# Optimization experiments

Hardware: AMD Instinct MI355X
Metric: run time of the kernel (lower is better)

The kernel has to match this reference:

```python
import jax, jax.numpy as jnp
import numpy as np

N, E, D = 40000, 320000, 128          # nodes, edges, model dim
H, C = 4, 128                          # GAT heads, per-head channels
DEPTH, MLP = 2, 512
NEG_SLOPE = 0.2
EPS_SM = 1e-16                         # PyG softmax denom epsilon


def layer_norm(x, g, b):
    mu = jnp.mean(x, axis=-1, keepdims=True)
    var = jnp.var(x, axis=-1, keepdims=True)
    return (x - mu) * jax.lax.rsqrt(var + 1e-5) * g + b


def gat_conv(x, src, dst, edge_attr, W, a_src, a_dst, We, a_edge, bias):
    # x: [N,D]; W: [D,H*C]; a_*: [H,C]; We: [1,H*C]; bias: [H*C]
    h = (x @ W).reshape(N, H, C)                       # [N,H,C]
    alpha_src = jnp.einsum('nhc,hc->nh', h, a_src)      # [N,H]
    alpha_dst = jnp.einsum('nhc,hc->nh', h, a_dst)      # [N,H]
    e = (edge_attr @ We).reshape(E, H, C)               # [E,H,C]
    alpha_e = jnp.einsum('ehc,hc->eh', e, a_edge)       # [E,H]
    alpha = alpha_src[src] + alpha_dst[dst] + alpha_e   # [E,H]
    alpha = jax.nn.leaky_relu(alpha, NEG_SLOPE)
    # segment softmax over edges sharing the same destination node
    amax = jax.ops.segment_max(alpha, dst, num_segments=N)   # [N,H]
    ex = jnp.exp(alpha - amax[dst])                          # [E,H]
    denom = jax.ops.segment_sum(ex, dst, num_segments=N)     # [N,H]
    attn = ex / (denom[dst] + EPS_SM)                        # [E,H]
    # message = attn * x_j ; aggregate by destination (scatter-add)
    msg = attn[:, :, None] * h[src]                          # [E,H,C]
    out = jax.ops.segment_sum(msg, dst, num_segments=N)      # [N,H,C]
    return out.reshape(N, H * C) + bias                      # concat heads


def setup_inputs():
    key = jax.random.key(0)
    ks = jax.random.split(key, 16)
    s = 0.05
    f32 = jnp.float32
    inp = {
        'x': jax.random.normal(ks[0], (N, D), f32),
        'edge_index': jax.random.randint(ks[1], (2, E), 0, N),
        'edge_attr': jax.random.normal(ks[2], (E, 1), f32),
        'ln1_g': jnp.ones((DEPTH, D), f32),
        'ln1_b': jnp.zeros((DEPTH, D), f32),
        'gat_W': jax.random.normal(ks[3], (DEPTH, D, H * C), f32) * s,
        'att_src': jax.random.normal(ks[4], (DEPTH, H, C), f32) * s,
        'att_dst': jax.random.normal(ks[5], (DEPTH, H, C), f32) * s,
        'edge_W': jax.random.normal(ks[6], (DEPTH, 1, H * C), f32) * s,
        'att_edge': jax.random.normal(ks[7], (DEPTH, H, C), f32) * s,
        'gat_bias': jnp.zeros((DEPTH, H * C), f32),
        'qf_W': jax.random.normal(ks[8], (DEPTH, H * C, D), f32) * s,
        'qf_b': jnp.zeros((DEPTH, D), f32),
        'ln2_g': jnp.ones((DEPTH, D), f32),
        'ln2_b': jnp.zeros((DEPTH, D), f32),
        'ff_W1': jax.random.normal(ks[9], (DEPTH, D, MLP), f32) * s,
        'ff_b1': jnp.zeros((DEPTH, MLP), f32),
        'ff_W2': jax.random.normal(ks[10], (DEPTH, MLP, D), f32) * s,
        'ff_b2': jnp.zeros((DEPTH, D), f32),
    }
    return inp


def reference(x, edge_index, edge_attr, ln1_g, ln1_b, gat_W, att_src, att_dst,
              edge_W, att_edge, gat_bias, qf_W, qf_b, ln2_g, ln2_b,
              ff_W1, ff_b1, ff_W2, ff_b2):
    src, dst = edge_index[0], edge_index[1]
    for d in range(DEPTH):
        # Residual(PreNorm(QuickFix(GATConv)))
        h = layer_norm(x, ln1_g[d], ln1_b[d])
        g = gat_conv(h, src, dst, edge_attr, gat_W[d], att_src[d], att_dst[d],
                     edge_W[d], att_edge[d], gat_bias[d])
        x = x + g @ qf_W[d] + qf_b[d]
        # Residual(PreNorm(FeedForward))
        h = layer_norm(x, ln2_g[d], ln2_b[d])
        x = x + jax.nn.gelu(h @ ff_W1[d] + ff_b1[d]) @ ff_W2[d] + ff_b2[d]
    return x
```

## Files before the change

kernel.cpp:

```cpp
#include <hip/hip_runtime.h>
#include <hip/hip_bf16.h>

#define N_NODES 40000
#define M_PAD   40064
#define N_EDGES 320000
#define DIM 128
#define HC 512
#define NHEAD 4
#define CHEAD 128
#define DEPTH_L 2
#define MLP_DIM 512
#define SCAN_NB ((N_NODES + 255) / 256)

typedef __attribute__((ext_vector_type(8))) short short8;
typedef __attribute__((ext_vector_type(4))) float f32x4;

static __device__ __forceinline__ void gload_lds16(const void* g, void* l)
{
    __builtin_amdgcn_global_load_lds(
        (const __attribute__((address_space(1))) unsigned int*)g,
        (__attribute__((address_space(3))) unsigned int*)l,
        16, 0, 0);
}

static __device__ __forceinline__ unsigned int packbf2(float a, float b)
{
    union { __hip_bfloat16 h[2]; unsigned int u; } p;
    p.h[0] = __float2bfloat16(a);
    p.h[1] = __float2bfloat16(b);
    return p.u;
}

static __device__ __forceinline__ float gelu_f(float v)
{
    float z2 = -1.5957691216f * (v + 0.044715f * v * v * v);
    return v / (1.f + __expf(z2));
}

__global__ __launch_bounds__(256) void k_ln(const float* __restrict__ x,
                                            const float* __restrict__ gma,
                                            const float* __restrict__ bta,
                                            __hip_bfloat16* __restrict__ out, int M)
{
    int row = blockIdx.x * 4 + (threadIdx.x >> 6);
    int lane = threadIdx.x & 63;
    if (row >= M) return;
    float2 v = *reinterpret_cast<const float2*>(x + (size_t)row * DIM + lane * 2);
    float s = v.x + v.y, sq = v.x * v.x + v.y * v.y;
    #pragma unroll
    for (int d = 32; d; d >>= 1) { s += __shfl_xor(s, d); sq += __shfl_xor(sq, d); }
    float mean = s * (1.f / DIM);
    float var = sq * (1.f / DIM) - mean * mean;
    float rs = rsqrtf(var + 1e-5f);
    int c = lane * 2;
    union { __hip_bfloat16 b[2]; unsigned int u; } p;
    p.b[0] = __float2bfloat16((v.x - mean) * rs * gma[c] + bta[c]);
    p.b[1] = __float2bfloat16((v.y - mean) * rs * gma[c + 1] + bta[c + 1]);
    *reinterpret_cast<unsigned int*>(out + (size_t)row * DIM + c) = p.u;
}

struct WcvtArgs {
    const float* src[4];
    __hip_bfloat16* dst[4];
    int K[4];
    int Nn[4];
};
__global__ __launch_bounds__(256) void k_wcvt4(WcvtArgs a)
{
    int j = blockIdx.y;
    int i = blockIdx.x * 256 + threadIdx.x;
    int K = a.K[j], N = a.Nn[j];
    if (i < K * N) {
        int n = i / K, k = i % K;
        a.dst[j][i] = __float2bfloat16(a.src[j][(size_t)k * N + n]);
    }
}

__global__ void k_prep_u(const float* __restrict__ gat_W,
                         const float* __restrict__ att_src,
                         const float* __restrict__ att_dst,
                         float* __restrict__ uvec)
{
    int b = blockIdx.x;
    int d = b >> 3, t8 = b & 7;
    int t = t8 >> 2, h = t8 & 3;
    int c = threadIdx.x;
    const float* W = gat_W + (size_t)d * DIM * HC;
    const float* av = (t == 0 ? att_src : att_dst) + (size_t)d * NHEAD * CHEAD + h * CHEAD;
    float s = 0.f;
    for (int cc = 0; cc < CHEAD; ++cc)
        s += W[(size_t)c * HC + h * CHEAD + cc] * av[cc];
    uvec[(size_t)d * 1024 + t8 * 128 + c] = s;
}

__global__ __launch_bounds__(256) void k_prep_m(const float* __restrict__ gat_W,
                                                const float* __restrict__ qf_W,
                                                __hip_bfloat16* __restrict__ Mt)
{
    int i = blockIdx.x * 256 + threadIdx.x;
    int d = i >> 16;
    int hk = (i >> 7) & 511;
    int j = i & 127;
    int h = hk >> 7, k = hk & 127;
    const float* W = gat_W + (size_t)d * DIM * HC + (size_t)k * HC + h * CHEAD;
    const float* Q = qf_W + (size_t)d * HC * DIM + (size_t)h * CHEAD * DIM + j;
    float s = 0.f;
    for (int c = 0; c < CHEAD; ++c)
        s += W[c] * Q[(size_t)c * DIM];
    Mt[(size_t)d * 65536 + (size_t)j * 512 + hk] = __float2bfloat16(s);
}

__global__ __launch_bounds__(256) void k_prep_c(const float* __restrict__ gat_bias,
                                                const float* __restrict__ qf_W,
                                                const float* __restrict__ qf_b,
                                                float* __restrict__ cvec)
{
    int idx = blockIdx.x * 4 + (threadIdx.x >> 6);
    int lane = threadIdx.x & 63;
    int d = idx >> 7, j = idx & 127;
    float s = 0.f;
    for (int m = lane; m < HC; m += 64)
        s += gat_bias[(size_t)d * HC + m] * qf_W[(size_t)d * HC * DIM + (size_t)m * DIM + j];
    #pragma unroll
    for (int dd = 32; dd; dd >>= 1) s += __shfl_xor(s, dd);
    if (lane == 0) cvec[idx] = s + qf_b[(size_t)d * DIM + j];
}

__global__ void k_ae(const float* __restrict__ We, const float* __restrict__ a_edge,
                     float* __restrict__ ae)
{
    int d = blockIdx.x;
    int h = threadIdx.x >> 6, lane = threadIdx.x & 63;
    float2 w = *reinterpret_cast<const float2*>(We + (size_t)d * HC + h * CHEAD + lane * 2);
    float2 a = *reinterpret_cast<const float2*>(a_edge + (size_t)d * NHEAD * CHEAD + h * CHEAD + lane * 2);
    float s = w.x * a.x + w.y * a.y;
    #pragma unroll
    for (int dd = 32; dd; dd >>= 1) s += __shfl_xor(s, dd);
    if (lane == 0) ae[d * 4 + h] = s;
}

__global__ __launch_bounds__(256) void k_dots(const unsigned int* __restrict__ hln,
                                              const float* __restrict__ uvec,
                                              float* __restrict__ asrc,
                                              float* __restrict__ adst)
{
    int n = blockIdx.x * 4 + (threadIdx.x >> 6);
    int lane = threadIdx.x & 63;
    unsigned int u = hln[n * 64 + lane];
    float f0 = __uint_as_float(u << 16);
    float f1 = __uint_as_float(u & 0xffff0000u);
    float s[8];
    #pragma unroll
    for (int t = 0; t < 8; ++t) {
        float2 uv = *reinterpret_cast<const float2*>(uvec + t * 128 + lane * 2);
        s[t] = f0 * uv.x + f1 * uv.y;
    }
    #pragma unroll
    for (int d = 32; d; d >>= 1) {
        #pragma unroll
        for (int t = 0; t < 8; ++t) s[t] += __shfl_xor(s[t], d);
    }
    if (lane == 0) {
        reinterpret_cast<float4*>(asrc)[n] = make_float4(s[0], s[1], s[2], s[3]);
        reinterpret_cast<float4*>(adst)[n] = make_float4(s[4], s[5], s[6], s[7]);
    }
}

__global__ __launch_bounds__(256) void k_alpha(const int* __restrict__ scsr,
                                               const int* __restrict__ dcsr,
                                               const float* __restrict__ eacsr,
                                               const float* __restrict__ asrc,
                                               const float* __restrict__ adst,
                                               const float* __restrict__ ae4v,
                                               float* __restrict__ wcsr)
{
    int p = blockIdx.x * 256 + threadIdx.x;
    if (p >= N_EDGES) return;
    int s = scsr[p], dd = dcsr[p];
    float q = eacsr[p];
    float4 as = reinterpret_cast<const float4*>(asrc)[s];
    float4 ad = reinterpret_cast<const float4*>(adst)[dd];
    float4 ae = *reinterpret_cast<const float4*>(ae4v);
    float4 w;
    float al;
    al = as.x + ad.x + ae.x * q; al = al > 0.f ? al : 0.2f * al; w.x = __expf(al);
    al = as.y + ad.y + ae.y * q; al = al > 0.f ? al : 0.2f * al; w.y = __expf(al);
    al = as.z + ad.z + ae.z * q; al = al > 0.f ? al : 0.2f * al; w.z = __expf(al);
    al = as.w + ad.w + ae.w * q; al = al > 0.f ? al : 0.2f * al; w.w = __expf(al);
    reinterpret_cast<float4*>(wcsr)[p] = w;
}

__global__ __launch_bounds__(256) void k_agg2(const int* __restrict__ off,
                                              const int* __restrict__ scsr,
                                              const float* __restrict__ wcsr,
                                              const unsigned int* __restrict__ hln,
                                              unsigned int* __restrict__ agg)
{
    int n = blockIdx.x * 4 + (threadIdx.x >> 6);
    int lane = threadIdx.x & 63;
    int e0 = off[n], e1 = off[n + 1];
    float den[4] = {0, 0, 0, 0};
    float accA[4] = {0, 0, 0, 0};
    float accB[4] = {0, 0, 0, 0};
    int i = e0;
    for (; i + 1 < e1; i += 2) {
        int s0 = scsr[i], s1 = scsr[i + 1];
        float4 w0 = reinterpret_cast<const float4*>(wcsr)[i];
        float4 w1 = reinterpret_cast<const float4*>(wcsr)[i + 1];
        unsigned int u0 = hln[s0 * 64 + lane];
        unsigned int u1 = hln[s1 * 64 + lane];
        float f00 = __uint_as_float(u0 << 16);
        float f01 = __uint_as_float(u0 & 0xffff0000u);
        float f10 = __uint_as_float(u1 << 16);
        float f11 = __uint_as_float(u1 & 0xffff0000u);
        den[0] += w0.x + w1.x; den[1] += w0.y + w1.y;
        den[2] += w0.z + w1.z; den[3] += w0.w + w1.w;
        accA[0] += w0.x * f00 + w1.x * f10; accB[0] += w0.x * f01 + w1.x * f11;
        accA[1] += w0.y * f00 + w1.y * f10; accB[1] += w0.y * f01 + w1.y * f11;
        accA[2] += w0.z * f00 + w1.z * f10; accB[2] += w0.z * f01 + w1.z * f11;
        accA[3] += w0.w * f00 + w1.w * f10; accB[3] += w0.w * f01 + w1.w * f11;
    }
    if (i < e1) {
        int s0 = scsr[i];
        float4 w0 = reinterpret_cast<const float4*>(wcsr)[i];
        unsigned int u0 = hln[s0 * 64 + lane];
        float f00 = __uint_as_float(u0 << 16);
        float f01 = __uint_as_float(u0 & 0xffff0000u);
        den[0] += w0.x; den[1] += w0.y; den[2] += w0.z; den[3] += w0.w;
        accA[0] += w0.x * f00; accB[0] += w0.x * f01;
        accA[1] += w0.y * f00; accB[1] += w0.y * f01;
        accA[2] += w0.z * f00; accB[2] += w0.z * f01;
        accA[3] += w0.w * f00; accB[3] += w0.w * f01;
    }
    #pragma unroll
    for (int h = 0; h < 4; ++h) {
        float inv = 1.f / (den[h] + 1e-16f);
        agg[n * 256 + h * 64 + lane] = packbf2(accA[h] * inv, accB[h] * inv);
    }
}

template <bool LN>
__global__ __launch_bounds__(256) void k_qf(const short* __restrict__ A,
                                            const short* __restrict__ Bt,
                                            const float* __restrict__ bias,
                                            const float* __restrict__ resid,
                                            float* __restrict__ xout,
                                            const float* __restrict__ gma,
                                            const float* __restrict__ bta,
                                            __hip_bfloat16* __restrict__ hout,
                                            int M)
{
    __shared__ __align__(16) short Bls[2][128 * 64];
    const int tid = threadIdx.x;
    const int lane = tid & 63;
    const int w = tid >> 6;
    const int lrow = lane & 15;
    const int lk = lane >> 4;
    const int mw = blockIdx.x * 64 + w * 16;

    auto stage = [&](int buf, int kt) {
        #pragma unroll
        for (int c0 = 0; c0 < 1024; c0 += 256) {
            int c = c0 + tid;
            int wb = c0 + (w << 6);
            int r = c >> 3, gq = c & 7, gp = gq ^ (r & 7);
            gload_lds16(Bt + (size_t)r * 512 + kt + gp * 8, &Bls[buf][wb * 8]);
        }
    };

    f32x4 acc[8] = {};
    stage(0, 0);
    __syncthreads();
    int cur = 0;
    for (int t = 0; t < 8; ++t) {
        if (t < 7) stage(cur ^ 1, (t + 1) * 64);
        #pragma unroll
        for (int ks = 0; ks < 2; ++ks) {
            short8 af = *reinterpret_cast<const short8*>(
                A + (size_t)(mw + lrow) * 512 + t * 64 + ks * 32 + lk * 8);
            short8 bf[8];
            #pragma unroll
            for (int fj = 0; fj < 8; ++fj) {
                int r = fj * 16 + lrow;
                int g = ks * 4 + lk;
                bf[fj] = *reinterpret_cast<const short8*>(
                    &Bls[cur][r * 64 + ((g ^ (r & 7)) * 8)]);
            }
            #pragma unroll
            for (int fj = 0; fj < 8; ++fj)
                acc[fj] = __builtin_amdgcn_mfma_f32_16x16x32_bf16(
                    af, bf[fj], acc[fj], 0, 0, 0);
        }
        __syncthreads();
        cur ^= 1;
    }

    #pragma unroll
    for (int p = 0; p < 4; ++p) {
        int m = mw + lk * 4 + p;
        float v[8], s = 0.f, sq = 0.f;
        #pragma unroll
        for (int fj = 0; fj < 8; ++fj) {
            int n = fj * 16 + lrow;
            v[fj] = acc[fj][p] + bias[n] + resid[(size_t)m * DIM + n];
            s += v[fj]; sq += v[fj] * v[fj];
        }
        #pragma unroll
        for (int fj = 0; fj < 8; ++fj)
            xout[(size_t)m * DIM + fj * 16 + lrow] = v[fj];
        if (LN) {
            #pragma unroll
            for (int d = 1; d < 16; d <<= 1) {
                s += __shfl_xor(s, d);
                sq += __shfl_xor(sq, d);
            }
            float mean = s * (1.f / DIM);
            float var = sq * (1.f / DIM) - mean * mean;
            float rs = rsqrtf(var + 1e-5f);
            #pragma unroll
            for (int fj = 0; fj < 8; ++fj) {
                int n = fj * 16 + lrow;
                hout[(size_t)m * DIM + n] =
                    __float2bfloat16((v[fj] - mean) * rs * gma[n] + bta[n]);
            }
        }
    }
}

template <bool LN>
__global__ __launch_bounds__(256) void k_ff(const short* __restrict__ A,
                                            const short* __restrict__ W1t,
                                            const short* __restrict__ W2t,
                                            const float* __restrict__ b1,
                                            const float* __restrict__ b2,
                                            const float* __restrict__ resid,
                                            float* __restrict__ xout,
                                            const float* __restrict__ gma,
                                            const float* __restrict__ bta,
                                            __hip_bfloat16* __restrict__ hout,
                                            int M)
{
    __shared__ __align__(16) short B1ls[64 * 128];
    __shared__ __align__(16) short B2ls[128 * 64];
    __shared__ __align__(16) short midls[4][16 * 64];
    const int tid = threadIdx.x;
    const int lane = tid & 63;
    const int w = tid >> 6;
    const int lrow = lane & 15;
    const int lk = lane >> 4;
    const int mw = blockIdx.x * 64 + w * 16;
    __hip_bfloat16* midw = (__hip_bfloat16*)midls[w];

    short8 af[4];
    #pragma unroll
    for (int ks = 0; ks < 4; ++ks)
        af[ks] = *reinterpret_cast<const short8*>(
            A + (size_t)(mw + lrow) * 128 + ks * 32 + lk * 8);

    auto stage1 = [&](int mc) {
        #pragma unroll
        for (int c0 = 0; c0 < 1024; c0 += 256) {
            int c = c0 + tid;
            int wb = c0 + (w << 6);
            int r = c >> 4, gq = c & 15, gp = gq ^ (r & 15);
            gload_lds16(W1t + (size_t)(mc * 64 + r) * 128 + gp * 8, &B1ls[wb * 8]);
        }
    };
    auto stage2 = [&](int mc) {
        #pragma unroll
        for (int c0 = 0; c0 < 1024; c0 += 256) {
            int c = c0 + tid;
            int wb = c0 + (w << 6);
            int r = c >> 3, gq = c & 7, gp = gq ^ (r & 7);
            gload_lds16(W2t + (size_t)r * 512 + mc * 64 + gp * 8, &B2ls[wb * 8]);
        }
    };

    f32x4 acc2[8] = {};
    stage1(0);
    for (int mc = 0; mc < 8; ++mc) {
        __syncthreads();
        stage2(mc);
        f32x4 acc1[4] = {};
        #pragma unroll
        for (int ks = 0; ks < 4; ++ks) {
            short8 bf1[4];
            #pragma unroll
            for (int fj = 0; fj < 4; ++fj) {
                int r = fj * 16 + lrow;
                bf1[fj] = *reinterpret_cast<const short8*>(
                    &B1ls[r * 128 + (((ks * 4 + lk) ^ (r & 15)) * 8)]);
            }
            #pragma unroll
            for (int fj = 0; fj < 4; ++fj)
                acc1[fj] = __builtin_amdgcn_mfma_f32_16x16x32_bf16(
                    af[ks], bf1[fj], acc1[fj], 0, 0, 0);
        }
        #pragma unroll
        for (int fj = 0; fj < 4; ++fj) {
            #pragma unroll
            for (int p = 0; p < 4; ++p) {
                int mloc = lk * 4 + p;
                int cloc = fj * 16 + lrow;
                float v = gelu_f(acc1[fj][p] + b1[mc * 64 + cloc]);
                int slot = (cloc >> 3) ^ (mloc & 7);
                midw[mloc * 64 + slot * 8 + (cloc & 7)] = __float2bfloat16(v);
            }
        }
        __syncthreads();
        if (mc < 7) stage1(mc + 1);
        #pragma unroll
        for (int ks2 = 0; ks2 < 2; ++ks2) {
            int g = ks2 * 4 + lk;
            short8 a2 = *reinterpret_cast<const short8*>(
                &midls[w][lrow * 64 + ((g ^ (lrow & 7)) * 8)]);
            short8 bf2[8];
            #pragma unroll
            for (int fj = 0; fj < 8; ++fj) {
                int r = fj * 16 + lrow;
                bf2[fj] = *reinterpret_cast<const short8*>(
                    &B2ls[r * 64 + (((g ^ (r & 7))) * 8)]);
            }
            #pragma unroll
            for (int fj = 0; fj < 8; ++fj)
                acc2[fj] = __builtin_amdgcn_mfma_f32_16x16x32_bf16(
                    a2, bf2[fj], acc2[fj], 0, 0, 0);
        }
    }

    #pragma unroll
    for (int p = 0; p < 4; ++p) {
        int m = mw + lk * 4 + p;
        float v[8], s = 0.f, sq = 0.f;
        #pragma unroll
        for (int fj = 0; fj < 8; ++fj) {
            int n = fj * 16 + lrow;
            v[fj] = acc2[fj][p] + b2[n] + resid[(size_t)m * DIM + n];
            s += v[fj]; sq += v[fj] * v[fj];
        }
        #pragma unroll
        for (int fj = 0; fj < 8; ++fj)
            xout[(size_t)m * DIM + fj * 16 + lrow] = v[fj];
        if (LN) {
            #pragma unroll
            for (int d = 1; d < 16; d <<= 1) {
                s += __shfl_xor(s, d);
                sq += __shfl_xor(sq, d);
            }
            float mean = s * (1.f / DIM);
            float var = sq * (1.f / DIM) - mean * mean;
            float rs = rsqrtf(var + 1e-5f);
            #pragma unroll
            for (int fj = 0; fj < 8; ++fj) {
                int n = fj * 16 + lrow;
                hout[(size_t)m * DIM + n] =
                    __float2bfloat16((v[fj] - mean) * rs * gma[n] + bta[n]);
            }
        }
    }
}

__global__ void k_hist(const int* __restrict__ dst, int* __restrict__ deg)
{
    int e = blockIdx.x * 256 + threadIdx.x;
    if (e < N_EDGES) atomicAdd(&deg[dst[e]], 1);
}

__global__ __launch_bounds__(256) void k_scan1(const int* __restrict__ deg,
                                               int* __restrict__ off,
                                               int* __restrict__ bsum)
{
    __shared__ int wsum[4];
    int b = blockIdx.x;
    int t = threadIdx.x, lane = t & 63, w = t >> 6;
    int i = b * 256 + t;
    int v = (i < N_NODES) ? deg[i] : 0;
    int s = v;
    #pragma unroll
    for (int d = 1; d < 64; d <<= 1) {
        int u = __shfl_up(s, d);
        if (lane >= d) s += u;
    }
    if (lane == 63) wsum[w] = s;
    __syncthreads();
    int wpre = 0;
    #pragma unroll
    for (int j = 0; j < 4; ++j)
        if (j < w) wpre += wsum[j];
    if (i < N_NODES) off[i] = wpre + s - v;
    if (t == 255) bsum[b] = wpre + s;
}

__global__ __launch_bounds__(256) void k_scan2(int* __restrict__ bsum,
                                               int* __restrict__ bpre)
{
    __shared__ int wsum[4];
    int t = threadIdx.x, lane = t & 63, w = t >> 6;
    int v = (t < SCAN_NB) ? bsum[t] : 0;
    int s = v;
    #pragma unroll
    for (int d = 1; d < 64; d <<= 1) {
        int u = __shfl_up(s, d);
        if (lane >= d) s += u;
    }
    if (lane == 63) wsum[w] = s;
    __syncthreads();
    int wpre = 0;
    #pragma unroll
    for (int j = 0; j < 4; ++j)
        if (j < w) wpre += wsum[j];
    if (t < SCAN_NB) bpre[t] = wpre + s - v;
    if (t == 255) bpre[SCAN_NB] = wpre + s;
}

__global__ __launch_bounds__(256) void k_scan3(int* __restrict__ off,
                                               const int* __restrict__ bpre,
                                               int* __restrict__ cur)
{
    int b = blockIdx.x;
    int i = b * 256 + threadIdx.x;
    if (i < N_NODES) {
        int o = off[i] + bpre[b];
        off[i] = o;
        cur[i] = o;
    }
    if (i == 0) off[N_NODES] = bpre[SCAN_NB];
}

__global__ void k_fill(const int* __restrict__ src, const int* __restrict__ dst,
                       const float* __restrict__ ea, int* __restrict__ cur,
                       int* __restrict__ scsr, int* __restrict__ dcsr,
                       float* __restrict__ eacsr)
{
    int e = blockIdx.x * 256 + threadIdx.x;
    if (e < N_EDGES) {
        int dd = dst[e];
        int p = atomicAdd(&cur[dd], 1);
        scsr[p] = src[e];
        dcsr[p] = dd;
        eacsr[p] = ea[e];
    }
}

extern "C" void kernel_launch(void* const* d_in, const int* in_sizes, int n_in,
                              void* d_out, int out_size, void* d_ws, size_t ws_size,
                              hipStream_t stream)
{
    const float* x_in     = (const float*)d_in[0];
    const int*   ei       = (const int*)d_in[1];
    const float* ea       = (const float*)d_in[2];
    const float* ln1_g    = (const float*)d_in[3];
    const float* ln1_b    = (const float*)d_in[4];
    const float* gat_W    = (const float*)d_in[5];
    const float* att_src  = (const float*)d_in[6];
    const float* att_dst  = (const float*)d_in[7];
    const float* edge_W   = (const float*)d_in[8];
    const float* att_edge = (const float*)d_in[9];
    const float* gat_bias = (const float*)d_in[10];
    const float* qf_W     = (const float*)d_in[11];
    const float* qf_b     = (const float*)d_in[12];
    const float* ln2_g    = (const float*)d_in[13];
    const float* ln2_b    = (const float*)d_in[14];
    const float* ff_W1    = (const float*)d_in[15];
    const float* ff_b1    = (const float*)d_in[16];
    const float* ff_W2    = (const float*)d_in[17];
    const float* ff_b2    = (const float*)d_in[18];
    float* x = (float*)d_out;

    char* ws = (char*)d_ws;
    size_t o = 0;
    auto alloc = [&](size_t b) { size_t r = o; o += (b + 255) & ~(size_t)255; return r; };
    __hip_bfloat16*  h_ln  = (__hip_bfloat16*)(ws + alloc((size_t)M_PAD * DIM * 2));
    __hip_bfloat16*  gbuf  = (__hip_bfloat16*)(ws + alloc((size_t)M_PAD * HC * 2));
    float*           asrc  = (float*)(ws + alloc((size_t)N_NODES * 4 * 4));
    float*           adst  = (float*)(ws + alloc((size_t)N_NODES * 4 * 4));
    float*           ae4   = (float*)(ws + alloc(256));
    float*           uvec  = (float*)(ws + alloc((size_t)DEPTH_L * 1024 * 4));
    __hip_bfloat16*  Mt    = (__hip_bfloat16*)(ws + alloc((size_t)DEPTH_L * 65536 * 2));
    float*           cvec  = (float*)(ws + alloc(256 * 4));
    int*             deg   = (int*)(ws + alloc((size_t)(N_NODES + 1) * 4));
    int*             off   = (int*)(ws + alloc((size_t)(N_NODES + 1) * 4));
    int*             cur   = (int*)(ws + alloc((size_t)N_NODES * 4));
    int*             bsum  = (int*)(ws + alloc((size_t)(SCAN_NB + 1) * 4));
    int*             bpre  = (int*)(ws + alloc((size_t)(SCAN_NB + 1) * 4));
    int*             scsr  = (int*)(ws + alloc((size_t)N_EDGES * 4));
    int*             dcsr  = (int*)(ws + alloc((size_t)N_EDGES * 4));
    float*           eacsr = (float*)(ws + alloc((size_t)N_EDGES * 4));
    float*           wcsr  = (float*)(ws + alloc((size_t)N_EDGES * 4 * 4));
    __hip_bfloat16* Wt[DEPTH_L][2];
    for (int d = 0; d < DEPTH_L; ++d)
        for (int j = 0; j < 2; ++j)
            Wt[d][j] = (__hip_bfloat16*)(ws + alloc((size_t)65536 * 2));

    const int* srcA = ei;
    const int* dstA = ei + N_EDGES;

    WcvtArgs wa;
    for (int d = 0; d < DEPTH_L; ++d) {
        wa.src[d * 2 + 0] = ff_W1 + (size_t)d * DIM * MLP_DIM; wa.K[d * 2 + 0] = DIM;     wa.Nn[d * 2 + 0] = MLP_DIM;
        wa.src[d * 2 + 1] = ff_W2 + (size_t)d * MLP_DIM * DIM; wa.K[d * 2 + 1] = MLP_DIM; wa.Nn[d * 2 + 1] = DIM;
        wa.dst[d * 2 + 0] = Wt[d][0];
        wa.dst[d * 2 + 1] = Wt[d][1];
    }
    k_wcvt4<<<dim3(256, 4), 256, 0, stream>>>(wa);
    k_prep_u<<<16, 128, 0, stream>>>(gat_W, att_src, att_dst, uvec);
    k_prep_m<<<512, 256, 0, stream>>>(gat_W, qf_W, Mt);
    k_prep_c<<<64, 256, 0, stream>>>(gat_bias, qf_W, qf_b, cvec);
    k_ae<<<2, 256, 0, stream>>>(edge_W, att_edge, ae4);

    hipMemsetAsync(deg, 0, (size_t)(N_NODES + 1) * 4, stream);
    k_hist<<<(N_EDGES + 255) / 256, 256, 0, stream>>>(dstA, deg);
    k_scan1<<<SCAN_NB, 256, 0, stream>>>(deg, off, bsum);
    k_scan2<<<1, 256, 0, stream>>>(bsum, bpre);
    k_scan3<<<SCAN_NB, 256, 0, stream>>>(off, bpre, cur);
    k_fill<<<(N_EDGES + 255) / 256, 256, 0, stream>>>(srcA, dstA, ea, cur, scsr, dcsr, eacsr);

    const int QB = N_NODES / 64;
    const int NB = N_NODES / 4;
    const int EB = (N_EDGES + 255) / 256;

    k_ln<<<NB, 256, 0, stream>>>(x_in, ln1_g, ln1_b, h_ln, N_NODES);
    k_dots<<<NB, 256, 0, stream>>>((const unsigned int*)h_ln, uvec, asrc, adst);

    for (int d = 0; d < DEPTH_L; ++d) {
        const float* resid0 = (d == 0) ? x_in : x;
        k_alpha<<<EB, 256, 0, stream>>>(scsr, dcsr, eacsr, asrc, adst, ae4 + d * 4, wcsr);
        k_agg2<<<NB, 256, 0, stream>>>(off, scsr, wcsr, (const unsigned int*)h_ln,
            (unsigned int*)gbuf);
        k_qf<true><<<QB, 256, 0, stream>>>((const short*)gbuf,
            (const short*)(Mt + (size_t)d * 65536), cvec + d * 128, resid0, x,
            ln2_g + d * DIM, ln2_b + d * DIM, h_ln, N_NODES);
        if (d + 1 < DEPTH_L) {
            k_ff<true><<<QB, 256, 0, stream>>>((const short*)h_ln,
                (const short*)Wt[d][0], (const short*)Wt[d][1],
                ff_b1 + d * MLP_DIM, ff_b2 + d * DIM, x, x,
                ln1_g + (d + 1) * DIM, ln1_b + (d + 1) * DIM, h_ln, N_NODES);
            k_dots<<<NB, 256, 0, stream>>>((const unsigned int*)h_ln,
                uvec + (size_t)(d + 1) * 1024, asrc, adst);
        } else {
            k_ff<false><<<QB, 256, 0, stream>>>((const short*)h_ln,
                (const short*)Wt[d][0], (const short*)Wt[d][1],
                ff_b1 + d * MLP_DIM, ff_b2 + d * DIM, x, x,
                nullptr, nullptr, nullptr, N_NODES);
        }
    }
}
```

Before: 295.9 us.

## Fuse QuickFix projection and feed-forward into one per-layer kernel

```diff
diff --git a/kernel.cpp b/kernel.cpp
--- a/kernel.cpp
+++ b/kernel.cpp
@@ -2,7 +2,6 @@
 #include <hip/hip_bf16.h>
 
 #define N_NODES 40000
-#define M_PAD   40064
 #define N_EDGES 320000
 #define DIM 128
 #define HC 512
@@ -239,18 +238,26 @@
     }
 }
 
-template <bool LN>
-__global__ __launch_bounds__(256) void k_qf(const short* __restrict__ A,
-                                            const short* __restrict__ Bt,
-                                            const float* __restrict__ bias,
-                                            const float* __restrict__ resid,
-                                            float* __restrict__ xout,
-                                            const float* __restrict__ gma,
-                                            const float* __restrict__ bta,
-                                            __hip_bfloat16* __restrict__ hout,
-                                            int M)
-{
-    __shared__ __align__(16) short Bls[2][128 * 64];
+template <bool LNN>
+__global__ __launch_bounds__(256) void k_layer(const short* __restrict__ A,
+                                               const short* __restrict__ Mt,
+                                               const float* __restrict__ cvec,
+                                               const float* __restrict__ resid,
+                                               const short* __restrict__ W1t,
+                                               const short* __restrict__ W2t,
+                                               const float* __restrict__ b1,
+                                               const float* __restrict__ b2,
+                                               const float* __restrict__ ln2g,
+                                               const float* __restrict__ ln2b,
+                                               const float* __restrict__ ln1g,
+                                               const float* __restrict__ ln1b,
+                                               float* __restrict__ xout,
+                                               __hip_bfloat16* __restrict__ hout,
+                                               int M)
+{
+    __shared__ __align__(16) short wst[2][8192];
+    __shared__ __align__(16) short w2st[2][8192];
+    __shared__ __align__(16) short scratch[8192];
     const int tid = threadIdx.x;
     const int lane = tid & 63;
     const int w = tid >> 6;
@@ -258,57 +265,172 @@
     const int lk = lane >> 4;
     const int mw = blockIdx.x * 64 + w * 16;
 
-    auto stage = [&](int buf, int kt) {
+    short8 aq[16];
+    #pragma unroll
+    for (int t = 0; t < 16; ++t)
+        aq[t] = *reinterpret_cast<const short8*>(
+            A + (size_t)(mw + lrow) * 512 + t * 32 + lk * 8);
+
+    auto stageQ = [&](int buf, int kt) {
         #pragma unroll
         for (int c0 = 0; c0 < 1024; c0 += 256) {
             int c = c0 + tid;
             int wb = c0 + (w << 6);
-            int r = c >> 3, gq = c & 7, gp = gq ^ (r & 7);
-            gload_lds16(Bt + (size_t)r * 512 + kt + gp * 8, &Bls[buf][wb * 8]);
+            int r = c >> 3, gp = (c & 7) ^ (r & 7);
+            gload_lds16(Mt + (size_t)r * 512 + kt + gp * 8, &wst[buf][wb * 8]);
         }
     };
 
-    f32x4 acc[8] = {};
-    stage(0, 0);
+    f32x4 accq[8] = {};
+    stageQ(0, 0);
     __syncthreads();
-    int cur = 0;
+    #pragma unroll
     for (int t = 0; t < 8; ++t) {
-        if (t < 7) stage(cur ^ 1, (t + 1) * 64);
+        if (t < 7) stageQ((t & 1) ^ 1, (t + 1) * 64);
         #pragma unroll
         for (int ks = 0; ks < 2; ++ks) {
-            short8 af = *reinterpret_cast<const short8*>(
-                A + (size_t)(mw + lrow) * 512 + t * 64 + ks * 32 + lk * 8);
+            short8 af = aq[t * 2 + ks];
             short8 bf[8];
             #pragma unroll
             for (int fj = 0; fj < 8; ++fj) {
                 int r = fj * 16 + lrow;
                 int g = ks * 4 + lk;
                 bf[fj] = *reinterpret_cast<const short8*>(
-                    &Bls[cur][r * 64 + ((g ^ (r & 7)) * 8)]);
+                    &wst[t & 1][r * 64 + ((g ^ (r & 7)) * 8)]);
             }
             #pragma unroll
             for (int fj = 0; fj < 8; ++fj)
-                acc[fj] = __builtin_amdgcn_mfma_f32_16x16x32_bf16(
-                    af, bf[fj], acc[fj], 0, 0, 0);
+                accq[fj] = __builtin_amdgcn_mfma_f32_16x16x32_bf16(
+                    af, bf[fj], accq[fj], 0, 0, 0);
         }
         __syncthreads();
-        cur ^= 1;
-    }
-
+    }
+
+    auto stage1 = [&](int buf, int mc) {
+        #pragma unroll
+        for (int c0 = 0; c0 < 1024; c0 += 256) {
+            int c = c0 + tid;
+            int wb = c0 + (w << 6);
+            int r = c >> 4, gp = (c & 15) ^ (r & 15);
+            gload_lds16(W1t + (size_t)(mc * 64 + r) * 128 + gp * 8, &wst[buf][wb * 8]);
+        }
+    };
+    auto stage2 = [&](int buf, int mc) {
+        #pragma unroll
+        for (int c0 = 0; c0 < 1024; c0 += 256) {
+            int c = c0 + tid;
+            int wb = c0 + (w << 6);
+            int r = c >> 3, gp = (c & 7) ^ (r & 7);
+            gload_lds16(W2t + (size_t)r * 512 + mc * 64 + gp * 8, &w2st[buf][wb * 8]);
+        }
+    };
+    stage1(0, 0);
+    stage2(0, 0);
+
+    short* scr_w = scratch + w * 2048;
+    float xv[4][8];
     #pragma unroll
     for (int p = 0; p < 4; ++p) {
         int m = mw + lk * 4 + p;
-        float v[8], s = 0.f, sq = 0.f;
+        int mloc = lk * 4 + p;
+        float s = 0.f, sq = 0.f;
         #pragma unroll
         for (int fj = 0; fj < 8; ++fj) {
             int n = fj * 16 + lrow;
-            v[fj] = acc[fj][p] + bias[n] + resid[(size_t)m * DIM + n];
-            s += v[fj]; sq += v[fj] * v[fj];
-        }
-        #pragma unroll
-        for (int fj = 0; fj < 8; ++fj)
-            xout[(size_t)m * DIM + fj * 16 + lrow] = v[fj];
-        if (LN) {
+            float v = accq[fj][p] + cvec[n] + resid[(size_t)m * DIM + n];
+            xv[p][fj] = v; s += v; sq += v * v;
+        }
+        #pragma unroll
+        for (int d = 1; d < 16; d <<= 1) {
+            s += __shfl_xor(s, d);
+            sq += __shfl_xor(sq, d);
+        }
+        float mean = s * (1.f / DIM);
+        float var = sq * (1.f / DIM) - mean * mean;
+        float rs = rsqrtf(var + 1e-5f);
+        #pragma unroll
+        for (int fj = 0; fj < 8; ++fj) {
+            int c = fj * 16 + lrow;
+            float h = (xv[p][fj] - mean) * rs * ln2g[c] + ln2b[c];
+            int g = c >> 3;
+            ((__hip_bfloat16*)scr_w)[mloc * 128 + ((g ^ mloc) & 15) * 8 + (c & 7)] =
+                __float2bfloat16(h);
+        }
+    }
+    short8 af2[4];
+    #pragma unroll
+    for (int ks = 0; ks < 4; ++ks) {
+        int g = ks * 4 + lk;
+        af2[ks] = *reinterpret_cast<const short8*>(
+            &scr_w[lrow * 128 + ((g ^ lrow) * 8)]);
+    }
+
+    __hip_bfloat16* midw = (__hip_bfloat16*)(scratch + w * 1024);
+    f32x4 acc2[8] = {};
+    #pragma unroll
+    for (int mc = 0; mc < 8; ++mc) {
+        __syncthreads();
+        if (mc < 7) {
+            stage1((mc & 1) ^ 1, mc + 1);
+            stage2((mc & 1) ^ 1, mc + 1);
+        }
+        f32x4 acc1[4] = {};
+        #pragma unroll
+        for (int ks = 0; ks < 4; ++ks) {
+            short8 bf1[4];
+            #pragma unroll
+            for (int fj = 0; fj < 4; ++fj) {
+                int r = fj * 16 + lrow;
+                bf1[fj] = *reinterpret_cast<const short8*>(
+                    &wst[mc & 1][r * 128 + (((ks * 4 + lk) ^ (r & 15)) * 8)]);
+            }
+            #pragma unroll
+            for (int fj = 0; fj < 4; ++fj)
+                acc1[fj] = __builtin_amdgcn_mfma_f32_16x16x32_bf16(
+                    af2[ks], bf1[fj], acc1[fj], 0, 0, 0);
+        }
+        #pragma unroll
+        for (int fj = 0; fj < 4; ++fj) {
+            #pragma unroll
+            for (int p = 0; p < 4; ++p) {
+                int mloc = lk * 4 + p;
+                int cloc = fj * 16 + lrow;
+                float v = gelu_f(acc1[fj][p] + b1[mc * 64 + cloc]);
+                int slot = (cloc >> 3) ^ (mloc & 7);
+                midw[mloc * 64 + slot * 8 + (cloc & 7)] = __float2bfloat16(v);
+            }
+        }
+        #pragma unroll
+        for (int ks2 = 0; ks2 < 2; ++ks2) {
+            int g = ks2 * 4 + lk;
+            short8 a2 = *reinterpret_cast<const short8*>(
+                &((short*)midw)[lrow * 64 + ((g ^ (lrow & 7)) * 8)]);
+            short8 bf2[8];
+            #pragma unroll
+            for (int fj = 0; fj < 8; ++fj) {
+                int r = fj * 16 + lrow;
+                bf2[fj] = *reinterpret_cast<const short8*>(
+                    &w2st[mc & 1][r * 64 + ((g ^ (r & 7)) * 8)]);
+            }
+            #pragma unroll
+            for (int fj = 0; fj < 8; ++fj)
+                acc2[fj] = __builtin_amdgcn_mfma_f32_16x16x32_bf16(
+                    a2, bf2[fj], acc2[fj], 0, 0, 0);
+        }
+    }
+
+    #pragma unroll
+    for (int p = 0; p < 4; ++p) {
+        int m = mw + lk * 4 + p;
+        float s = 0.f, sq = 0.f;
+        #pragma unroll
+        for (int fj = 0; fj < 8; ++fj) {
+            int n = fj * 16 + lrow;
+            float v = xv[p][fj] + acc2[fj][p] + b2[n];
+            xv[p][fj] = v; s += v; sq += v * v;
+            xout[(size_t)m * DIM + n] = v;
+        }
+        if (LNN) {
             #pragma unroll
             for (int d = 1; d < 16; d <<= 1) {
                 s += __shfl_xor(s, d);
@@ -321,140 +443,7 @@
             for (int fj = 0; fj < 8; ++fj) {
                 int n = fj * 16 + lrow;
                 hout[(size_t)m * DIM + n] =
-                    __float2bfloat16((v[fj] - mean) * rs * gma[n] + bta[n]);
-            }
-        }
-    }
-}
-
-template <bool LN>
-__global__ __launch_bounds__(256) void k_ff(const short* __restrict__ A,
-                                            const short* __restrict__ W1t,
-                                            const short* __restrict__ W2t,
-                                            const float* __restrict__ b1,
-                                            const float* __restrict__ b2,
-                                            const float* __restrict__ resid,
-                                            float* __restrict__ xout,
-                                            const float* __restrict__ gma,
-                                            const float* __restrict__ bta,
-                                            __hip_bfloat16* __restrict__ hout,
-                                            int M)
-{
-    __shared__ __align__(16) short B1ls[64 * 128];
-    __shared__ __align__(16) short B2ls[128 * 64];
-    __shared__ __align__(16) short midls[4][16 * 64];
-    const int tid = threadIdx.x;
-    const int lane = tid & 63;
-    const int w = tid >> 6;
-    const int lrow = lane & 15;
-    const int lk = lane >> 4;
-    const int mw = blockIdx.x * 64 + w * 16;
-    __hip_bfloat16* midw = (__hip_bfloat16*)midls[w];
-
-    short8 af[4];
-    #pragma unroll
-    for (int ks = 0; ks < 4; ++ks)
-        af[ks] = *reinterpret_cast<const short8*>(
-            A + (size_t)(mw + lrow) * 128 + ks * 32 + lk * 8);
-
-    auto stage1 = [&](int mc) {
-        #pragma unroll
-        for (int c0 = 0; c0 < 1024; c0 += 256) {
-            int c = c0 + tid;
-            int wb = c0 + (w << 6);
-            int r = c >> 4, gq = c & 15, gp = gq ^ (r & 15);
-            gload_lds16(W1t + (size_t)(mc * 64 + r) * 128 + gp * 8, &B1ls[wb * 8]);
-        }
-    };
-    auto stage2 = [&](int mc) {
-        #pragma unroll
-        for (int c0 = 0; c0 < 1024; c0 += 256) {
-            int c = c0 + tid;
-            int wb = c0 + (w << 6);
-            int r = c >> 3, gq = c & 7, gp = gq ^ (r & 7);
-            gload_lds16(W2t + (size_t)r * 512 + mc * 64 + gp * 8, &B2ls[wb * 8]);
-        }
-    };
-
-    f32x4 acc2[8] = {};
-    stage1(0);
-    for (int mc = 0; mc < 8; ++mc) {
-        __syncthreads();
-        stage2(mc);
-        f32x4 acc1[4] = {};
-        #pragma unroll
-        for (int ks = 0; ks < 4; ++ks) {
-            short8 bf1[4];
-            #pragma unroll
-            for (int fj = 0; fj < 4; ++fj) {
-                int r = fj * 16 + lrow;
-                bf1[fj] = *reinterpret_cast<const short8*>(
-                    &B1ls[r * 128 + (((ks * 4 + lk) ^ (r & 15)) * 8)]);
-            }
-            #pragma unroll
-            for (int fj = 0; fj < 4; ++fj)
-                acc1[fj] = __builtin_amdgcn_mfma_f32_16x16x32_bf16(
-                    af[ks], bf1[fj], acc1[fj], 0, 0, 0);
-        }
-        #pragma unroll
-        for (int fj = 0; fj < 4; ++fj) {
-            #pragma unroll
-            for (int p = 0; p < 4; ++p) {
-                int mloc = lk * 4 + p;
-                int cloc = fj * 16 + lrow;
-                float v = gelu_f(acc1[fj][p] + b1[mc * 64 + cloc]);
-                int slot = (cloc >> 3) ^ (mloc & 7);
-                midw[mloc * 64 + slot * 8 + (cloc & 7)] = __float2bfloat16(v);
-            }
-        }
-        __syncthreads();
-        if (mc < 7) stage1(mc + 1);
-        #pragma unroll
-        for (int ks2 = 0; ks2 < 2; ++ks2) {
-            int g = ks2 * 4 + lk;
-            short8 a2 = *reinterpret_cast<const short8*>(
-                &midls[w][lrow * 64 + ((g ^ (lrow & 7)) * 8)]);
-            short8 bf2[8];
-            #pragma unroll
-            for (int fj = 0; fj < 8; ++fj) {
-                int r = fj * 16 + lrow;
-                bf2[fj] = *reinterpret_cast<const short8*>(
-                    &B2ls[r * 64 + (((g ^ (r & 7))) * 8)]);
-            }
-            #pragma unroll
-            for (int fj = 0; fj < 8; ++fj)
-                acc2[fj] = __builtin_amdgcn_mfma_f32_16x16x32_bf16(
-                    a2, bf2[fj], acc2[fj], 0, 0, 0);
-        }
-    }
-
-    #pragma unroll
-    for (int p = 0; p < 4; ++p) {
-        int m = mw + lk * 4 + p;
-        float v[8], s = 0.f, sq = 0.f;
-        #pragma unroll
-        for (int fj = 0; fj < 8; ++fj) {
-            int n = fj * 16 + lrow;
-            v[fj] = acc2[fj][p] + b2[n] + resid[(size_t)m * DIM + n];
-            s += v[fj]; sq += v[fj] * v[fj];
-        }
-        #pragma unroll
-        for (int fj = 0; fj < 8; ++fj)
-            xout[(size_t)m * DIM + fj * 16 + lrow] = v[fj];
-        if (LN) {
-            #pragma unroll
-            for (int d = 1; d < 16; d <<= 1) {
-                s += __shfl_xor(s, d);
-                sq += __shfl_xor(sq, d);
-            }
-            float mean = s * (1.f / DIM);
-            float var = sq * (1.f / DIM) - mean * mean;
-            float rs = rsqrtf(var + 1e-5f);
-            #pragma unroll
-            for (int fj = 0; fj < 8; ++fj) {
-                int n = fj * 16 + lrow;
-                hout[(size_t)m * DIM + n] =
-                    __float2bfloat16((v[fj] - mean) * rs * gma[n] + bta[n]);
+                    __float2bfloat16((xv[p][fj] - mean) * rs * ln1g[n] + ln1b[n]);
             }
         }
     }
@@ -570,8 +559,8 @@
     char* ws = (char*)d_ws;
     size_t o = 0;
     auto alloc = [&](size_t b) { size_t r = o; o += (b + 255) & ~(size_t)255; return r; };
-    __hip_bfloat16*  h_ln  = (__hip_bfloat16*)(ws + alloc((size_t)M_PAD * DIM * 2));
-    __hip_bfloat16*  gbuf  = (__hip_bfloat16*)(ws + alloc((size_t)M_PAD * HC * 2));
+    __hip_bfloat16*  h_ln  = (__hip_bfloat16*)(ws + alloc((size_t)N_NODES * DIM * 2));
+    __hip_bfloat16*  gbuf  = (__hip_bfloat16*)(ws + alloc((size_t)N_NODES * HC * 2));
     float*           asrc  = (float*)(ws + alloc((size_t)N_NODES * 4 * 4));
     float*           adst  = (float*)(ws + alloc((size_t)N_NODES * 4 * 4));
     float*           ae4   = (float*)(ws + alloc(256));
@@ -627,21 +616,24 @@
         k_alpha<<<EB, 256, 0, stream>>>(scsr, dcsr, eacsr, asrc, adst, ae4 + d * 4, wcsr);
         k_agg2<<<NB, 256, 0, stream>>>(off, scsr, wcsr, (const unsigned int*)h_ln,
             (unsigned int*)gbuf);
-        k_qf<true><<<QB, 256, 0, stream>>>((const short*)gbuf,
-            (const short*)(Mt + (size_t)d * 65536), cvec + d * 128, resid0, x,
-            ln2_g + d * DIM, ln2_b + d * DIM, h_ln, N_NODES);
         if (d + 1 < DEPTH_L) {
-            k_ff<true><<<QB, 256, 0, stream>>>((const short*)h_ln,
+            k_layer<true><<<QB, 256, 0, stream>>>((const short*)gbuf,
+                (const short*)(Mt + (size_t)d * 65536), cvec + d * 128, resid0,
                 (const short*)Wt[d][0], (const short*)Wt[d][1],
-                ff_b1 + d * MLP_DIM, ff_b2 + d * DIM, x, x,
-                ln1_g + (d + 1) * DIM, ln1_b + (d + 1) * DIM, h_ln, N_NODES);
+                ff_b1 + d * MLP_DIM, ff_b2 + d * DIM,
+                ln2_g + d * DIM, ln2_b + d * DIM,
+                ln1_g + (d + 1) * DIM, ln1_b + (d + 1) * DIM,
+                x, h_ln, N_NODES);
             k_dots<<<NB, 256, 0, stream>>>((const unsigned int*)h_ln,
                 uvec + (size_t)(d + 1) * 1024, asrc, adst);
         } else {
-            k_ff<false><<<QB, 256, 0, stream>>>((const short*)h_ln,
+            k_layer<false><<<QB, 256, 0, stream>>>((const short*)gbuf,
+                (const short*)(Mt + (size_t)d * 65536), cvec + d * 128, resid0,
                 (const short*)Wt[d][0], (const short*)Wt[d][1],
-                ff_b1 + d * MLP_DIM, ff_b2 + d * DIM, x, x,
-                nullptr, nullptr, nullptr, N_NODES);
-        }
-    }
-}
+                ff_b1 + d * MLP_DIM, ff_b2 + d * DIM,
+                ln2_g + d * DIM, ln2_b + d * DIM,
+                nullptr, nullptr,
+                x, nullptr, N_NODES);
+        }
+    }
+}
```

Result: slower. 313.6 us (+6.0%).
